# Kernel tuning notes

Hardware: AMD Instinct MI355X
Metric: run time of the kernel (lower is better)

## Reference

```python
import jax, jax.numpy as jnp
import numpy as np

B, V, NFEAT, INTER, NHID1, NHID12, NCLASS = 131072, 8, 32, 8, 16, 8, 2


def setup_inputs() -> dict:
    key = jax.random.key(0)
    ks = jax.random.split(key, 16)
    # node feature tensor: channel 0 = node type in {0,1}, channels 1..32 = features
    types = jax.random.randint(ks[0], (B, V, 1), 0, 2).astype(jnp.float32)
    feats = jax.random.normal(ks[1], (B, V, NFEAT), dtype=jnp.float32)
    x = jnp.concatenate([types, feats], axis=-1)  # (B, V, 33)
    adj = jax.random.uniform(ks[2], (B, V, V), dtype=jnp.float32)
    edge_attr = jax.random.normal(ks[3], (B, V, V), dtype=jnp.float32)
    s = lambda k, *sh: jax.random.normal(k, sh, dtype=jnp.float32) * 0.1
    return {
        "x": x, "adj": adj, "edge_attr": edge_attr,
        "wa": s(ks[4], INTER, NFEAT), "ba": jnp.zeros((INTER,), jnp.float32),
        "wb": s(ks[5], INTER, NFEAT), "bb": jnp.zeros((INTER,), jnp.float32),
        "w1": s(ks[6], NFEAT, NHID1), "b1": jnp.zeros((NHID1,), jnp.float32),
        "w2": s(ks[7], NHID1, NHID12), "b2": jnp.zeros((NHID12,), jnp.float32),
        "wg": s(ks[8], NHID12, NHID12), "bg": jnp.zeros((NHID12,), jnp.float32),
        "wf": s(ks[9], NCLASS, NHID12), "bf": jnp.zeros((NCLASS,), jnp.float32),
    }


def _attn_pool(h, wg, bg):
    # GlobalAttentionPooling: softmax(gate_nn(h)) over nodes, weighted sum
    gate = jax.nn.softmax(jnp.einsum('bvc,oc->bvo', h, wg) + bg, axis=1)
    return jnp.sum(gate * h, axis=1)  # (B, NHID12)


def reference(x, adj, edge_attr, wa, ba, wb, bb, w1, b1, w2, b2, wg, bg, wf, bf):
    node_types = x[..., 0]           # (B, V)
    feat = x[..., 1:]                # (B, V, 32)
    # conv_b (1x1 conv == per-node linear), output layout (B, inter, V)
    Fk = jnp.einsum('bvc,oc->bov', feat, wb) + bb[None, :, None]  # (B, 8, V=8)
    S = jax.nn.softmax(jnp.matmul(Fk, Fk), axis=1)                # (B, 8, 8)
    W = adj * (S + edge_attr)                                     # (B, V, V)
    # graph conv 1: (W @ feat) @ w1 + b1, LeakyReLU(0.01)
    h = jax.nn.leaky_relu(jnp.einsum('bvw,bwc->bvc', W, feat) @ w1 + b1)
    # graph conv 2
    h = jax.nn.leaky_relu(jnp.einsum('bvw,bwc->bvc', W, h) @ w2 + b2)  # (B, V, 8)
    # per-type masked attention pooling; types fixed to {0, 1}
    pooled = []
    for t in (0.0, 1.0):
        mask = (node_types == t)[..., None].astype(h.dtype)
        pooled.append(_attn_pool(h * mask, wg, bg))
    x_pool = jnp.mean(jnp.stack(pooled, axis=1), axis=1)  # (B, NHID12)
    return x_pool @ wf.T + bf  # (B, NCLASS)
```

## Files before the change

kernel.cpp:

```cpp
#include <hip/hip_runtime.h>


#define SLOTS 16
#define NTHREADS 128

typedef float4 __attribute__((aligned(4))) f4u;

__device__ __forceinline__ float grp_sum8(float x) {
    x += __shfl_xor(x, 1);
    x += __shfl_xor(x, 2);
    x += __shfl_xor(x, 4);
    return x;
}
__device__ __forceinline__ void wavefence() { __builtin_amdgcn_wave_barrier(); }

__global__ __launch_bounds__(NTHREADS, 4)
void gcn_fused(const float* __restrict__ x,
               const float* __restrict__ adj,
               const float* __restrict__ edge,
               const float* __restrict__ wb, const float* __restrict__ bb,
               const float* __restrict__ w1, const float* __restrict__ b1,
               const float* __restrict__ w2, const float* __restrict__ b2,
               const float* __restrict__ wg, const float* __restrict__ bg,
               const float* __restrict__ wf, const float* __restrict__ bf,
               float* __restrict__ out, int Btot)
{
    __shared__ float bufA[SLOTS * 72];
    __shared__ float bufB[SLOTS * 136];

    const int tid  = threadIdx.x;
    const int slot = tid >> 3;
    const int v    = tid & 7;
    long long bb_ = (long long)blockIdx.x * SLOTS + slot;
    if (bb_ >= Btot) bb_ = Btot - 1;
    const size_t b = (size_t)bb_;

    float* A  = &bufA[slot * 72];
    float* Bg = &bufB[slot * 136];

    const float4* ar = (const float4*)(adj  + b * 64 + (size_t)v * 8);
    const float4* er = (const float4*)(edge + b * 64 + (size_t)v * 8);
    const float4 a0 = ar[0], a1 = ar[1];
    const float4 e0 = er[0], e1 = er[1];

    const float* xr = x + b * 264 + (size_t)v * 33;
    const float type = xr[0];
    const f4u* xq = (const f4u*)(xr + 1);
    float4 q[8];
#pragma unroll
    for (int k = 0; k < 8; ++k) q[k] = xq[k];

    float Fk[8];
#pragma unroll
    for (int o = 0; o < 8; ++o) Fk[o] = bb[o];
    float g1[16];
#pragma unroll
    for (int j = 0; j < 16; ++j) g1[j] = 0.f;
#pragma unroll
    for (int k = 0; k < 8; ++k) {
        const float f[4] = { q[k].x, q[k].y, q[k].z, q[k].w };
#pragma unroll
        for (int u = 0; u < 4; ++u) {
            const int c = 4 * k + u;
            const float fv = f[u];
#pragma unroll
            for (int o = 0; o < 8; ++o) Fk[o] += fv * wb[o * 32 + c];
#pragma unroll
            for (int j = 0; j < 16; ++j) g1[j] += fv * w1[c * 16 + j];
        }
    }

#pragma unroll
    for (int o = 0; o < 8; ++o) A[o * 8 + v] = Fk[o];
    {
        float4* gp = (float4*)(Bg + v * 16);
        gp[0] = make_float4(g1[0],  g1[1],  g1[2],  g1[3]);
        gp[1] = make_float4(g1[4],  g1[5],  g1[6],  g1[7]);
        gp[2] = make_float4(g1[8],  g1[9],  g1[10], g1[11]);
        gp[3] = make_float4(g1[12], g1[13], g1[14], g1[15]);
    }
    wavefence();

    float M[8];
#pragma unroll
    for (int o = 0; o < 8; ++o) {
        const float4* fr = (const float4*)(A + o * 8);
        const float4 r0 = fr[0], r1 = fr[1];
        M[o] = r0.x * Fk[0] + r0.y * Fk[1] + r0.z * Fk[2] + r0.w * Fk[3]
             + r1.x * Fk[4] + r1.y * Fk[5] + r1.z * Fk[6] + r1.w * Fk[7];
    }
    wavefence();
    float mx = M[0];
#pragma unroll
    for (int o = 1; o < 8; ++o) mx = fmaxf(mx, M[o]);
    float ssum = 0.f;
#pragma unroll
    for (int o = 0; o < 8; ++o) { M[o] = __expf(M[o] - mx); ssum += M[o]; }
    const float sinv = 1.f / ssum;
#pragma unroll
    for (int o = 0; o < 8; ++o) A[o * 8 + v] = M[o] * sinv;
    wavefence();

    const float4* sr = (const float4*)(A + v * 8);
    const float4 s0 = sr[0], s1 = sr[1];
    float W[8];
    W[0] = a0.x * (s0.x + e0.x);  W[1] = a0.y * (s0.y + e0.y);
    W[2] = a0.z * (s0.z + e0.z);  W[3] = a0.w * (s0.w + e0.w);
    W[4] = a1.x * (s1.x + e1.x);  W[5] = a1.y * (s1.y + e1.y);
    W[6] = a1.z * (s1.z + e1.z);  W[7] = a1.w * (s1.w + e1.w);

    float msg1[16];
#pragma unroll
    for (int j = 0; j < 16; ++j) msg1[j] = 0.f;
#pragma unroll
    for (int w = 0; w < 8; ++w) {
        const float wv = W[w];
        const float4* gp = (const float4*)(Bg + w * 16);
        const float4 q0 = gp[0], q1 = gp[1], q2 = gp[2], q3 = gp[3];
        msg1[0]  += wv * q0.x; msg1[1]  += wv * q0.y; msg1[2]  += wv * q0.z; msg1[3]  += wv * q0.w;
        msg1[4]  += wv * q1.x; msg1[5]  += wv * q1.y; msg1[6]  += wv * q1.z; msg1[7]  += wv * q1.w;
        msg1[8]  += wv * q2.x; msg1[9]  += wv * q2.y; msg1[10] += wv * q2.z; msg1[11] += wv * q2.w;
        msg1[12] += wv * q3.x; msg1[13] += wv * q3.y; msg1[14] += wv * q3.z; msg1[15] += wv * q3.w;
    }
    float h[16];
#pragma unroll
    for (int j = 0; j < 16; ++j) {
        const float t = msg1[j] + b1[j];
        h[j] = t > 0.f ? t : 0.01f * t;
    }

    float g2[8];
#pragma unroll
    for (int n = 0; n < 8; ++n) g2[n] = 0.f;
#pragma unroll
    for (int j = 0; j < 16; ++j) {
        const float hv = h[j];
#pragma unroll
        for (int n = 0; n < 8; ++n) g2[n] += hv * w2[j * 8 + n];
    }
    wavefence();
    {
        float4* gp = (float4*)(A + v * 8);
        gp[0] = make_float4(g2[0], g2[1], g2[2], g2[3]);
        gp[1] = make_float4(g2[4], g2[5], g2[6], g2[7]);
    }
    wavefence();

    float msg2[8];
#pragma unroll
    for (int n = 0; n < 8; ++n) msg2[n] = 0.f;
#pragma unroll
    for (int w = 0; w < 8; ++w) {
        const float wv = W[w];
        const float4* gp = (const float4*)(A + w * 8);
        const float4 q0 = gp[0], q1 = gp[1];
        msg2[0] += wv * q0.x; msg2[1] += wv * q0.y; msg2[2] += wv * q0.z; msg2[3] += wv * q0.w;
        msg2[4] += wv * q1.x; msg2[5] += wv * q1.y; msg2[6] += wv * q1.z; msg2[7] += wv * q1.w;
    }
    float h2[8];
#pragma unroll
    for (int n = 0; n < 8; ++n) {
        const float t = msg2[n] + b2[n];
        h2[n] = t > 0.f ? t : 0.01f * t;
    }
    wavefence();

#pragma unroll
    for (int n = 0; n < 8; ++n) A[v * 9 + n] = h2[n];
    A[v * 9 + 8] = type;
    wavefence();

    const int o = v;
    float d[8], ty[8], ho[8];
#pragma unroll
    for (int vp = 0; vp < 8; ++vp) {
        const float* hr = A + vp * 9;
        float acc = 0.f;
#pragma unroll
        for (int n = 0; n < 8; ++n) acc += hr[n] * wg[o * 8 + n];
        d[vp] = acc;
        ty[vp] = hr[8];
        ho[vp] = hr[o];
    }
    float xp = 0.f;
#pragma unroll
    for (int t = 0; t < 2; ++t) {
        const float tv = (float)t;
        float l[8];
        float lmx = -1e30f;
#pragma unroll
        for (int vp = 0; vp < 8; ++vp) {
            l[vp] = (ty[vp] == tv) ? d[vp] : 0.f;
            lmx = fmaxf(lmx, l[vp]);
        }
        float esum = 0.f, num = 0.f;
#pragma unroll
        for (int vp = 0; vp < 8; ++vp) {
            const float e = __expf(l[vp] - lmx);
            esum += e;
            num  += (ty[vp] == tv) ? e * ho[vp] : 0.f;
        }
        xp += 0.5f * num / esum;
    }

    const float y0 = grp_sum8(xp * wf[0 * 8 + o]);
    const float y1 = grp_sum8(xp * wf[1 * 8 + o]);
    if (v == 0) {
        float2* op = (float2*)(out + b * 2);
        *op = make_float2(y0 + bf[0], y1 + bf[1]);
    }
}

extern "C" void kernel_launch(void* const* d_in, const int* in_sizes, int n_in,
                              void* d_out, int out_size, void* d_ws, size_t ws_size,
                              hipStream_t stream) {
    const float* x    = (const float*)d_in[0];
    const float* adj  = (const float*)d_in[1];
    const float* edge = (const float*)d_in[2];
    const float* wb   = (const float*)d_in[5];
    const float* bb   = (const float*)d_in[6];
    const float* w1   = (const float*)d_in[7];
    const float* b1   = (const float*)d_in[8];
    const float* w2   = (const float*)d_in[9];
    const float* b2   = (const float*)d_in[10];
    const float* wg   = (const float*)d_in[11];
    const float* bg   = (const float*)d_in[12];
    const float* wf   = (const float*)d_in[13];
    const float* bf   = (const float*)d_in[14];
    float* out = (float*)d_out;

    const int Btot = in_sizes[0] / 264;
    const int grid = (Btot + SLOTS - 1) / SLOTS;

    gcn_fused<<<grid, NTHREADS, 0, stream>>>(x, adj, edge, wb, bb, w1, b1,
                                             w2, b2, wg, bg, wf, bf, out, Btot);
}
```

Baseline: 301.3 us.

## Use persistent grid-stride blocks with register prefetch of next graph's features

Launches a fixed grid of up to 2048 blocks that loop over groups of 16 graphs. Each iteration prefetches the next group's node features into registers so the global load overlaps current compute. It also computes the gate projection per node before the pooling exchange instead of after it, which removes the redundant per-thread 8x8 dot products. The cost is higher register pressure from the prefetch buffer, which may lower occupancy, and the bounds clamp for a partial last group has been dropped.

```diff
diff --git a/kernel.cpp b/kernel.cpp
--- a/kernel.cpp
+++ b/kernel.cpp
@@ -3,6 +3,7 @@
 
 #define SLOTS 16
 #define NTHREADS 128
+#define NBLOCKS 2048
 
 typedef float4 __attribute__((aligned(4))) f4u;
 
@@ -23,7 +24,7 @@
                const float* __restrict__ w2, const float* __restrict__ b2,
                const float* __restrict__ wg, const float* __restrict__ bg,
                const float* __restrict__ wf, const float* __restrict__ bf,
-               float* __restrict__ out, int Btot)
+               float* __restrict__ out, int nGroups)
 {
     __shared__ float bufA[SLOTS * 72];
     __shared__ float bufB[SLOTS * 136];
@@ -31,183 +32,214 @@
     const int tid  = threadIdx.x;
     const int slot = tid >> 3;
     const int v    = tid & 7;
-    long long bb_ = (long long)blockIdx.x * SLOTS + slot;
-    if (bb_ >= Btot) bb_ = Btot - 1;
-    const size_t b = (size_t)bb_;
-
     float* A  = &bufA[slot * 72];
     float* Bg = &bufB[slot * 136];
 
-    const float4* ar = (const float4*)(adj  + b * 64 + (size_t)v * 8);
-    const float4* er = (const float4*)(edge + b * 64 + (size_t)v * 8);
-    const float4 a0 = ar[0], a1 = ar[1];
-    const float4 e0 = er[0], e1 = er[1];
-
-    const float* xr = x + b * 264 + (size_t)v * 33;
-    const float type = xr[0];
-    const f4u* xq = (const f4u*)(xr + 1);
-    float4 q[8];
-#pragma unroll
-    for (int k = 0; k < 8; ++k) q[k] = xq[k];
-
-    float Fk[8];
-#pragma unroll
-    for (int o = 0; o < 8; ++o) Fk[o] = bb[o];
-    float g1[16];
-#pragma unroll
-    for (int j = 0; j < 16; ++j) g1[j] = 0.f;
-#pragma unroll
-    for (int k = 0; k < 8; ++k) {
-        const float f[4] = { q[k].x, q[k].y, q[k].z, q[k].w };
-#pragma unroll
-        for (int u = 0; u < 4; ++u) {
-            const int c = 4 * k + u;
-            const float fv = f[u];
-#pragma unroll
-            for (int o = 0; o < 8; ++o) Fk[o] += fv * wb[o * 32 + c];
-#pragma unroll
-            for (int j = 0; j < 16; ++j) g1[j] += fv * w1[c * 16 + j];
-        }
+    const int stride = gridDim.x;
+
+    float ntype; float4 nq[8];
+    {
+        const size_t nb = (size_t)blockIdx.x * SLOTS + slot;
+        const float* xr = x + nb * 264 + (size_t)v * 33;
+        ntype = xr[0];
+        const f4u* xq = (const f4u*)(xr + 1);
+#pragma unroll
+        for (int k = 0; k < 8; ++k) nq[k] = xq[k];
     }
 
-#pragma unroll
-    for (int o = 0; o < 8; ++o) A[o * 8 + v] = Fk[o];
-    {
-        float4* gp = (float4*)(Bg + v * 16);
-        gp[0] = make_float4(g1[0],  g1[1],  g1[2],  g1[3]);
-        gp[1] = make_float4(g1[4],  g1[5],  g1[6],  g1[7]);
-        gp[2] = make_float4(g1[8],  g1[9],  g1[10], g1[11]);
-        gp[3] = make_float4(g1[12], g1[13], g1[14], g1[15]);
-    }
-    wavefence();
-
-    float M[8];
-#pragma unroll
-    for (int o = 0; o < 8; ++o) {
-        const float4* fr = (const float4*)(A + o * 8);
-        const float4 r0 = fr[0], r1 = fr[1];
-        M[o] = r0.x * Fk[0] + r0.y * Fk[1] + r0.z * Fk[2] + r0.w * Fk[3]
-             + r1.x * Fk[4] + r1.y * Fk[5] + r1.z * Fk[6] + r1.w * Fk[7];
-    }
-    wavefence();
-    float mx = M[0];
-#pragma unroll
-    for (int o = 1; o < 8; ++o) mx = fmaxf(mx, M[o]);
-    float ssum = 0.f;
-#pragma unroll
-    for (int o = 0; o < 8; ++o) { M[o] = __expf(M[o] - mx); ssum += M[o]; }
-    const float sinv = 1.f / ssum;
-#pragma unroll
-    for (int o = 0; o < 8; ++o) A[o * 8 + v] = M[o] * sinv;
-    wavefence();
-
-    const float4* sr = (const float4*)(A + v * 8);
-    const float4 s0 = sr[0], s1 = sr[1];
-    float W[8];
-    W[0] = a0.x * (s0.x + e0.x);  W[1] = a0.y * (s0.y + e0.y);
-    W[2] = a0.z * (s0.z + e0.z);  W[3] = a0.w * (s0.w + e0.w);
-    W[4] = a1.x * (s1.x + e1.x);  W[5] = a1.y * (s1.y + e1.y);
-    W[6] = a1.z * (s1.z + e1.z);  W[7] = a1.w * (s1.w + e1.w);
-
-    float msg1[16];
-#pragma unroll
-    for (int j = 0; j < 16; ++j) msg1[j] = 0.f;
-#pragma unroll
-    for (int w = 0; w < 8; ++w) {
-        const float wv = W[w];
-        const float4* gp = (const float4*)(Bg + w * 16);
-        const float4 q0 = gp[0], q1 = gp[1], q2 = gp[2], q3 = gp[3];
-        msg1[0]  += wv * q0.x; msg1[1]  += wv * q0.y; msg1[2]  += wv * q0.z; msg1[3]  += wv * q0.w;
-        msg1[4]  += wv * q1.x; msg1[5]  += wv * q1.y; msg1[6]  += wv * q1.z; msg1[7]  += wv * q1.w;
-        msg1[8]  += wv * q2.x; msg1[9]  += wv * q2.y; msg1[10] += wv * q2.z; msg1[11] += wv * q2.w;
-        msg1[12] += wv * q3.x; msg1[13] += wv * q3.y; msg1[14] += wv * q3.z; msg1[15] += wv * q3.w;
-    }
-    float h[16];
-#pragma unroll
-    for (int j = 0; j < 16; ++j) {
-        const float t = msg1[j] + b1[j];
-        h[j] = t > 0.f ? t : 0.01f * t;
-    }
-
-    float g2[8];
-#pragma unroll
-    for (int n = 0; n < 8; ++n) g2[n] = 0.f;
-#pragma unroll
-    for (int j = 0; j < 16; ++j) {
-        const float hv = h[j];
-#pragma unroll
-        for (int n = 0; n < 8; ++n) g2[n] += hv * w2[j * 8 + n];
-    }
-    wavefence();
-    {
-        float4* gp = (float4*)(A + v * 8);
-        gp[0] = make_float4(g2[0], g2[1], g2[2], g2[3]);
-        gp[1] = make_float4(g2[4], g2[5], g2[6], g2[7]);
-    }
-    wavefence();
-
-    float msg2[8];
-#pragma unroll
-    for (int n = 0; n < 8; ++n) msg2[n] = 0.f;
-#pragma unroll
-    for (int w = 0; w < 8; ++w) {
-        const float wv = W[w];
-        const float4* gp = (const float4*)(A + w * 8);
-        const float4 q0 = gp[0], q1 = gp[1];
-        msg2[0] += wv * q0.x; msg2[1] += wv * q0.y; msg2[2] += wv * q0.z; msg2[3] += wv * q0.w;
-        msg2[4] += wv * q1.x; msg2[5] += wv * q1.y; msg2[6] += wv * q1.z; msg2[7] += wv * q1.w;
-    }
-    float h2[8];
-#pragma unroll
-    for (int n = 0; n < 8; ++n) {
-        const float t = msg2[n] + b2[n];
-        h2[n] = t > 0.f ? t : 0.01f * t;
-    }
-    wavefence();
-
-#pragma unroll
-    for (int n = 0; n < 8; ++n) A[v * 9 + n] = h2[n];
-    A[v * 9 + 8] = type;
-    wavefence();
-
-    const int o = v;
-    float d[8], ty[8], ho[8];
-#pragma unroll
-    for (int vp = 0; vp < 8; ++vp) {
-        const float* hr = A + vp * 9;
-        float acc = 0.f;
-#pragma unroll
-        for (int n = 0; n < 8; ++n) acc += hr[n] * wg[o * 8 + n];
-        d[vp] = acc;
-        ty[vp] = hr[8];
-        ho[vp] = hr[o];
-    }
-    float xp = 0.f;
-#pragma unroll
-    for (int t = 0; t < 2; ++t) {
-        const float tv = (float)t;
-        float l[8];
-        float lmx = -1e30f;
+    for (int g = blockIdx.x; g < nGroups; g += stride) {
+        const size_t b = (size_t)g * SLOTS + slot;
+
+        const float type = ntype;
+        float4 q[8];
+#pragma unroll
+        for (int k = 0; k < 8; ++k) q[k] = nq[k];
+        {
+            int ng = g + stride; if (ng >= nGroups) ng = g;
+            const size_t nb = (size_t)ng * SLOTS + slot;
+            const float* xr = x + nb * 264 + (size_t)v * 33;
+            ntype = xr[0];
+            const f4u* xq = (const f4u*)(xr + 1);
+#pragma unroll
+            for (int k = 0; k < 8; ++k) nq[k] = xq[k];
+        }
+
+        wavefence();
+
+        float Fk[8];
+#pragma unroll
+        for (int o = 0; o < 8; ++o) Fk[o] = bb[o];
+        float g1[16];
+#pragma unroll
+        for (int j = 0; j < 16; ++j) g1[j] = 0.f;
+#pragma unroll
+        for (int k = 0; k < 8; ++k) {
+            const float f[4] = { q[k].x, q[k].y, q[k].z, q[k].w };
+#pragma unroll
+            for (int u = 0; u < 4; ++u) {
+                const int c = 4 * k + u;
+                const float fv = f[u];
+#pragma unroll
+                for (int o = 0; o < 8; ++o) Fk[o] += fv * wb[o * 32 + c];
+#pragma unroll
+                for (int j = 0; j < 16; ++j) g1[j] += fv * w1[c * 16 + j];
+            }
+        }
+
+        const float4* ar = (const float4*)(adj  + b * 64 + (size_t)v * 8);
+        const float4* er = (const float4*)(edge + b * 64 + (size_t)v * 8);
+        const float4 a0 = ar[0], a1 = ar[1];
+        const float4 e0 = er[0], e1 = er[1];
+
+#pragma unroll
+        for (int o = 0; o < 8; ++o) A[o * 8 + v] = Fk[o];
+        {
+            float4* gp = (float4*)(Bg + v * 16);
+            gp[0] = make_float4(g1[0],  g1[1],  g1[2],  g1[3]);
+            gp[1] = make_float4(g1[4],  g1[5],  g1[6],  g1[7]);
+            gp[2] = make_float4(g1[8],  g1[9],  g1[10], g1[11]);
+            gp[3] = make_float4(g1[12], g1[13], g1[14], g1[15]);
+        }
+        wavefence();
+
+        float M[8];
+#pragma unroll
+        for (int o = 0; o < 8; ++o) {
+            const float4* fr = (const float4*)(A + o * 8);
+            const float4 r0 = fr[0], r1 = fr[1];
+            M[o] = r0.x * Fk[0] + r0.y * Fk[1] + r0.z * Fk[2] + r0.w * Fk[3]
+                 + r1.x * Fk[4] + r1.y * Fk[5] + r1.z * Fk[6] + r1.w * Fk[7];
+        }
+        wavefence();
+        float mx = M[0];
+#pragma unroll
+        for (int o = 1; o < 8; ++o) mx = fmaxf(mx, M[o]);
+        float ssum = 0.f;
+#pragma unroll
+        for (int o = 0; o < 8; ++o) { M[o] = __expf(M[o] - mx); ssum += M[o]; }
+        const float sinv = 1.f / ssum;
+#pragma unroll
+        for (int o = 0; o < 8; ++o) A[o * 8 + v] = M[o] * sinv;
+        wavefence();
+
+        const float4* sr = (const float4*)(A + v * 8);
+        const float4 s0 = sr[0], s1 = sr[1];
+        float W[8];
+        W[0] = a0.x * (s0.x + e0.x);  W[1] = a0.y * (s0.y + e0.y);
+        W[2] = a0.z * (s0.z + e0.z);  W[3] = a0.w * (s0.w + e0.w);
+        W[4] = a1.x * (s1.x + e1.x);  W[5] = a1.y * (s1.y + e1.y);
+        W[6] = a1.z * (s1.z + e1.z);  W[7] = a1.w * (s1.w + e1.w);
+
+        float msg1[16];
+#pragma unroll
+        for (int j = 0; j < 16; ++j) msg1[j] = 0.f;
+#pragma unroll
+        for (int w = 0; w < 8; ++w) {
+            const float wv = W[w];
+            const float4* gp = (const float4*)(Bg + w * 16);
+            const float4 q0 = gp[0], q1 = gp[1], q2 = gp[2], q3 = gp[3];
+            msg1[0]  += wv * q0.x; msg1[1]  += wv * q0.y; msg1[2]  += wv * q0.z; msg1[3]  += wv * q0.w;
+            msg1[4]  += wv * q1.x; msg1[5]  += wv * q1.y; msg1[6]  += wv * q1.z; msg1[7]  += wv * q1.w;
+            msg1[8]  += wv * q2.x; msg1[9]  += wv * q2.y; msg1[10] += wv * q2.z; msg1[11] += wv * q2.w;
+            msg1[12] += wv * q3.x; msg1[13] += wv * q3.y; msg1[14] += wv * q3.z; msg1[15] += wv * q3.w;
+        }
+        float h[16];
+#pragma unroll
+        for (int j = 0; j < 16; ++j) {
+            const float t = msg1[j] + b1[j];
+            h[j] = t > 0.f ? t : 0.01f * t;
+        }
+
+        float g2[8];
+#pragma unroll
+        for (int n = 0; n < 8; ++n) g2[n] = 0.f;
+#pragma unroll
+        for (int j = 0; j < 16; ++j) {
+            const float hv = h[j];
+#pragma unroll
+            for (int n = 0; n < 8; ++n) g2[n] += hv * w2[j * 8 + n];
+        }
+        wavefence();
+        {
+            float4* gp = (float4*)(A + v * 8);
+            gp[0] = make_float4(g2[0], g2[1], g2[2], g2[3]);
+            gp[1] = make_float4(g2[4], g2[5], g2[6], g2[7]);
+        }
+        wavefence();
+
+        float msg2[8];
+#pragma unroll
+        for (int n = 0; n < 8; ++n) msg2[n] = 0.f;
+#pragma unroll
+        for (int w = 0; w < 8; ++w) {
+            const float wv = W[w];
+            const float4* gp = (const float4*)(A + w * 8);
+            const float4 q0 = gp[0], q1 = gp[1];
+            msg2[0] += wv * q0.x; msg2[1] += wv * q0.y; msg2[2] += wv * q0.z; msg2[3] += wv * q0.w;
+            msg2[4] += wv * q1.x; msg2[5] += wv * q1.y; msg2[6] += wv * q1.z; msg2[7] += wv * q1.w;
+        }
+        float h2[8];
+#pragma unroll
+        for (int n = 0; n < 8; ++n) {
+            const float t = msg2[n] + b2[n];
+            h2[n] = t > 0.f ? t : 0.01f * t;
+        }
+
+        float Y[8];
+#pragma unroll
+        for (int o = 0; o < 8; ++o) {
+            float acc = 0.f;
+#pragma unroll
+            for (int n = 0; n < 8; ++n) acc += h2[n] * wg[o * 8 + n];
+            Y[o] = acc;
+        }
+        wavefence();
+        {
+            float4* hp = (float4*)(A + v * 8);
+            hp[0] = make_float4(h2[0], h2[1], h2[2], h2[3]);
+            hp[1] = make_float4(h2[4], h2[5], h2[6], h2[7]);
+            float4* yp = (float4*)(Bg + v * 8);
+            yp[0] = make_float4(Y[0], Y[1], Y[2], Y[3]);
+            yp[1] = make_float4(Y[4], Y[5], Y[6], Y[7]);
+            Bg[64 + v] = type;
+        }
+        wavefence();
+
+        const int o = v;
+        float yc[8], hc[8], ty[8];
 #pragma unroll
         for (int vp = 0; vp < 8; ++vp) {
-            l[vp] = (ty[vp] == tv) ? d[vp] : 0.f;
-            lmx = fmaxf(lmx, l[vp]);
-        }
-        float esum = 0.f, num = 0.f;
-#pragma unroll
-        for (int vp = 0; vp < 8; ++vp) {
-            const float e = __expf(l[vp] - lmx);
-            esum += e;
-            num  += (ty[vp] == tv) ? e * ho[vp] : 0.f;
-        }
-        xp += 0.5f * num / esum;
-    }
-
-    const float y0 = grp_sum8(xp * wf[0 * 8 + o]);
-    const float y1 = grp_sum8(xp * wf[1 * 8 + o]);
-    if (v == 0) {
-        float2* op = (float2*)(out + b * 2);
-        *op = make_float2(y0 + bf[0], y1 + bf[1]);
+            yc[vp] = Bg[vp * 8 + o];
+            hc[vp] = A[vp * 8 + o];
+            ty[vp] = Bg[64 + vp];
+        }
+        float xp = 0.f;
+#pragma unroll
+        for (int t = 0; t < 2; ++t) {
+            const float tv = (float)t;
+            float l[8];
+            float lmx = -1e30f;
+#pragma unroll
+            for (int vp = 0; vp < 8; ++vp) {
+                l[vp] = (ty[vp] == tv) ? yc[vp] : 0.f;
+                lmx = fmaxf(lmx, l[vp]);
+            }
+            float esum = 0.f, num = 0.f;
+#pragma unroll
+            for (int vp = 0; vp < 8; ++vp) {
+                const float e = __expf(l[vp] - lmx);
+                esum += e;
+                num  += (ty[vp] == tv) ? e * hc[vp] : 0.f;
+            }
+            xp += 0.5f * num / esum;
+        }
+
+        const float y0 = grp_sum8(xp * wf[0 * 8 + o]);
+        const float y1 = grp_sum8(xp * wf[1 * 8 + o]);
+        if (v == 0) {
+            float2* op = (float2*)(out + b * 2);
+            *op = make_float2(y0 + bf[0], y1 + bf[1]);
+        }
     }
 }
 
@@ -229,9 +261,10 @@
     const float* bf   = (const float*)d_in[14];
     float* out = (float*)d_out;
 
-    const int Btot = in_sizes[0] / 264;
-    const int grid = (Btot + SLOTS - 1) / SLOTS;
+    const int Btot    = in_sizes[0] / 264;
+    const int nGroups = (Btot + SLOTS - 1) / SLOTS;
+    const int grid    = nGroups < NBLOCKS ? nGroups : NBLOCKS;
 
     gcn_fused<<<grid, NTHREADS, 0, stream>>>(x, adj, edge, wb, bb, w1, b1,
-                                             w2, b2, wg, bg, wf, bf, out, Btot);
+                                             w2, b2, wg, bg, wf, bf, out, nGroups);
 }
```

Result: slower. 595.2 us (+97.6%).
